# Performance work log

Measured on AMD Instinct MI355X. Metric: run time of the kernel, lower is better.

Reference implementation:

```python
import jax, jax.numpy as jnp
import numpy as np

B, L = 16, 1024
D_MODEL = 384
EXPAND = 2
D_INNER = EXPAND * D_MODEL  # 768
D_STATE = 16
D_CONV = 4
DT_RANK = (D_MODEL + 15) // 16  # 24


def _causal_conv(x, w, b):
    # x: (B,L,Di); w: (Di,K) depthwise kernel; b: (Di,). Causal: pad K-1 on the left.
    K = w.shape[1]
    Lx = x.shape[1]
    xp = jnp.pad(x, ((0, 0), (K - 1, 0), (0, 0)))
    out = sum(xp[:, k:k + Lx, :] * w[:, k] for k in range(K)) + b
    return out


def _selective_scan(u, delta, A, Bm, Cm, Dv):
    # u, delta: (B,L,Di); A: (Di,N); Bm, Cm: (B,L,N); Dv: (Di,)
    def step(h, inp):
        dt, bt, ct, ut = inp  # (B,Di),(B,N),(B,N),(B,Di)
        dA = jnp.exp(dt[..., None] * A)                     # (B,Di,N)
        h = h * dA + (dt * ut)[..., None] * bt[:, None, :]  # (B,Di,N)
        y = jnp.einsum('bdn,bn->bd', h, ct)
        return h, y

    h0 = jnp.zeros((u.shape[0], u.shape[2], A.shape[1]), u.dtype)
    xs = (delta.swapaxes(0, 1), Bm.swapaxes(0, 1), Cm.swapaxes(0, 1), u.swapaxes(0, 1))
    _, ys = jax.lax.scan(step, h0, xs)
    return ys.swapaxes(0, 1) + u * Dv


def _mamba_dir(xz, conv_w, conv_bias, xproj_w, dt_w, dt_b, A_log, Dv):
    xh, z = jnp.split(xz, 2, axis=-1)                 # each (B,L,Di)
    xh = jax.nn.silu(_causal_conv(xh, conv_w, conv_bias))
    dbc = xh @ xproj_w.T                              # (B,L,DT_RANK+2N)
    dt, Bm, Cm = jnp.split(dbc, [DT_RANK, DT_RANK + D_STATE], axis=-1)
    delta = jax.nn.softplus(dt @ dt_w.T + dt_b)       # (B,L,Di)
    A = -jnp.exp(A_log)                               # (Di,N)
    y = _selective_scan(xh, delta, A, Bm, Cm, Dv)
    return y * jax.nn.silu(z)


def setup_inputs():
    key = jax.random.key(0)
    ks = jax.random.split(key, 16)

    def rn(k, shape, s):
        return jax.random.normal(k, shape, dtype=jnp.float32) * s

    A_init = jnp.log(jnp.tile(jnp.arange(1, D_STATE + 1, dtype=jnp.float32), (D_INNER, 1)))
    return dict(
        x=rn(ks[0], (B, L, D_MODEL), 1.0),
        ln_w=jnp.ones((D_MODEL,), jnp.float32),
        ln_b=jnp.zeros((D_MODEL,), jnp.float32),
        in_proj_w=rn(ks[1], (2 * D_INNER, D_MODEL), 0.02),
        out_proj_w=rn(ks[2], (D_MODEL, D_INNER), 0.02),
        conv_w_fwd=rn(ks[3], (D_INNER, D_CONV), 0.2),
        conv_bias_fwd=jnp.zeros((D_INNER,), jnp.float32),
        xproj_w_fwd=rn(ks[4], (DT_RANK + 2 * D_STATE, D_INNER), 0.02),
        dt_w_fwd=rn(ks[5], (D_INNER, DT_RANK), 0.1),
        dt_b_fwd=jnp.full((D_INNER,), -4.0, jnp.float32),
        A_log_fwd=A_init,
        D_fwd=jnp.ones((D_INNER,), jnp.float32),
        conv_w_bwd=rn(ks[6], (D_INNER, D_CONV), 0.2),
        conv_bias_bwd=jnp.zeros((D_INNER,), jnp.float32),
        xproj_w_bwd=rn(ks[7], (DT_RANK + 2 * D_STATE, D_INNER), 0.02),
        dt_w_bwd=rn(ks[8], (D_INNER, DT_RANK), 0.1),
        dt_b_bwd=jnp.full((D_INNER,), -4.0, jnp.float32),
        A_log_bwd=A_init,
        D_bwd=jnp.ones((D_INNER,), jnp.float32),
    )


def reference(x, ln_w, ln_b, in_proj_w, out_proj_w,
              conv_w_fwd, conv_bias_fwd, xproj_w_fwd, dt_w_fwd, dt_b_fwd, A_log_fwd, D_fwd,
              conv_w_bwd, conv_bias_bwd, xproj_w_bwd, dt_w_bwd, dt_b_bwd, A_log_bwd, D_bwd):
    # LayerNorm
    mu = x.mean(-1, keepdims=True)
    var = ((x - mu) ** 2).mean(-1, keepdims=True)
    xn = (x - mu) / jnp.sqrt(var + 1e-5) * ln_w + ln_b
    # Shared input projection -> (B,L,2*Di)
    xz = xn @ in_proj_w.T
    # Forward-direction mamba branch
    out_f = _mamba_dir(xz, conv_w_fwd, conv_bias_fwd, xproj_w_fwd, dt_w_fwd, dt_b_fwd, A_log_fwd, D_fwd)
    # Backward-direction branch on sequence-flipped xz, flipped back (bimamba v2)
    out_r = _mamba_dir(xz[:, ::-1], conv_w_bwd, conv_bias_bwd, xproj_w_bwd, dt_w_bwd, dt_b_bwd, A_log_bwd, D_bwd)[:, ::-1]
    # Output projection + residual (drop_path=0 -> identity)
    return x + (out_f + out_r) @ out_proj_w.T
```

## Files before the change

kernel.cpp:

```cpp
#include <hip/hip_runtime.h>
#include <cstdint>
#include <cstddef>

#define BN_   16
#define LN_   1024
#define DM_   384
#define DI_   768
#define NS_   16
#define RDT_  24
#define NDBC_ 56
#define NDBCP 64
#define NC_   16
#define LC_   64

typedef unsigned short ushortT;
typedef short bf16x8 __attribute__((ext_vector_type(8)));
typedef float f32x4 __attribute__((ext_vector_type(4)));

typedef __attribute__((address_space(3))) uint32_t lds_u32_t;
typedef __attribute__((address_space(1))) const uint32_t glb_u32_t;

static __device__ __forceinline__ void stage16(const void* g, void* lds) {
    __builtin_amdgcn_global_load_lds(
        (glb_u32_t*)(uintptr_t)g,
        (lds_u32_t*)(uint32_t)(uintptr_t)lds,
        16, 0, 0);
}

static __device__ __forceinline__ float silu_f(float x) {
    return x / (1.0f + __expf(-x));
}
static __device__ __forceinline__ float softplus_f(float s) {
    return fmaxf(s, 0.0f) + __logf(1.0f + __expf(-fabsf(s)));
}
static __device__ __forceinline__ ushortT f2bf(float f) {
    union { float f; uint32_t u; } v; v.f = f;
    uint32_t u = v.u;
    uint32_t r = u + 0x7fffu + ((u >> 16) & 1u);
    return (ushortT)(r >> 16);
}
static __device__ __forceinline__ float bf2f(ushortT b) {
    union { uint32_t u; float f; } v; v.u = ((uint32_t)b) << 16;
    return v.f;
}

__global__ __launch_bounds__(256) void wconv_kernel(
    const float* __restrict__ w1, int n1, const float* __restrict__ w2, int n2,
    const float* __restrict__ xwf, const float* __restrict__ xwb,
    const float* __restrict__ dwf, const float* __restrict__ dwb,
    ushortT* __restrict__ o1, ushortT* __restrict__ o2,
    ushortT* __restrict__ oxf, ushortT* __restrict__ oxb,
    ushortT* __restrict__ odf, ushortT* __restrict__ odb)
{
    int i = blockIdx.x * 256 + threadIdx.x;
    if (i < n1) { o1[i] = f2bf(w1[i]); return; }
    i -= n1;
    if (i < n2) { o2[i] = f2bf(w2[i]); return; }
    i -= n2;
    const int nx = NDBCP * DI_;
    if (i < 2 * nx) {
        int which = i >= nx;
        int j = which ? (i - nx) : i;
        int row = j / DI_;
        const float* src = which ? xwb : xwf;
        ushortT* dst = which ? oxb : oxf;
        dst[j] = (row < NDBC_) ? f2bf(src[j]) : (ushortT)0;
        return;
    }
    i -= 2 * nx;
    const int nd = DI_ * 32;
    if (i < 2 * nd) {
        int which = i >= nd;
        int j = which ? (i - nd) : i;
        int row = j >> 5, col = j & 31;
        const float* src = which ? dwb : dwf;
        ushortT* dst = which ? odb : odf;
        dst[j] = (col < RDT_) ? f2bf(src[row * RDT_ + col]) : (ushortT)0;
    }
}

__global__ __launch_bounds__(256) void ln_kernel(
    const float* __restrict__ x, const float* __restrict__ w,
    const float* __restrict__ b, ushortT* __restrict__ xn,
    int row0, int nrows)
{
    int r = blockIdx.x * 4 + (threadIdx.x >> 6);
    if (r >= nrows) return;
    int lane = threadIdx.x & 63;
    const float* xr = x + (size_t)(row0 + r) * DM_;
    float v[6];
    float s = 0.0f;
#pragma unroll
    for (int i = 0; i < 6; i++) { v[i] = xr[lane + 64 * i]; s += v[i]; }
#pragma unroll
    for (int o = 32; o > 0; o >>= 1) s += __shfl_down(s, o, 64);
    s = __shfl(s, 0, 64);
    float mu = s * (1.0f / DM_);
    float q = 0.0f;
#pragma unroll
    for (int i = 0; i < 6; i++) { float d = v[i] - mu; q += d * d; }
#pragma unroll
    for (int o = 32; o > 0; o >>= 1) q += __shfl_down(q, o, 64);
    q = __shfl(q, 0, 64);
    float rstd = rsqrtf(q * (1.0f / DM_) + 1e-5f);
    ushortT* outp = xn + (size_t)r * DM_;
#pragma unroll
    for (int i = 0; i < 6; i++) {
        int c = lane + 64 * i;
        outp[c] = f2bf((v[i] - mu) * rstd * w[c] + b[c]);
    }
}

template <int BM, int BN, int WR, int WC, bool CAT, bool RES, bool OB>
__global__ __launch_bounds__(256) void gemm_mfma(
    const ushortT* __restrict__ Aa, const ushortT* __restrict__ Ab_,
    const ushortT* __restrict__ W, const float* __restrict__ R,
    void* __restrict__ Cv, int M, int N, int Khalf)
{
    constexpr int WTM = BM / WR;
    constexpr int WTN = BN / WC;
    constexpr int FM = WTM / 16;
    constexpr int FN = WTN / 16;
    __shared__ ushortT As[BM * 32];
    __shared__ ushortT Ws[BN * 32];
    int tid = threadIdx.x;
    int bm = blockIdx.x * BM, bn = blockIdx.y * BN;
    int wave = tid >> 6, lane = tid & 63;
    int wm = wave % WR, wn = wave / WR;
    f32x4 acc[FM][FN] = {};
    int Ktot = CAT ? 2 * Khalf : Khalf;
    int lrow = lane >> 2;
    int lk = (lane & 3) * 8;

    for (int k0 = 0; k0 < Ktot; k0 += 32) {
        const ushortT* Asrc = (!CAT || k0 < Khalf) ? Aa : Ab_;
        int ka = (!CAT || k0 < Khalf) ? k0 : (k0 - Khalf);
        __syncthreads();
#pragma unroll
        for (int c = 0; c < BM / 64; c++) {
            int ch = c * 4 + wave;
            int row = ch * 16 + lrow;
            stage16(Asrc + (size_t)(bm + row) * Khalf + ka + lk, &As[ch * 16 * 32]);
        }
#pragma unroll
        for (int c = 0; c < BN / 64; c++) {
            int ch = c * 4 + wave;
            int row = ch * 16 + lrow;
            stage16(W + (size_t)(bn + row) * Khalf + ka + lk, &Ws[ch * 16 * 32]);
        }
        __syncthreads();
        int mb = (wm * WTM + (lane & 15)) * 32 + (lane >> 4) * 8;
        int nb = (wn * WTN + (lane & 15)) * 32 + (lane >> 4) * 8;
        bf16x8 af[FM], bfr[FN];
#pragma unroll
        for (int mi = 0; mi < FM; mi++) af[mi] = *(bf16x8*)&As[mb + mi * 16 * 32];
#pragma unroll
        for (int ni = 0; ni < FN; ni++) bfr[ni] = *(bf16x8*)&Ws[nb + ni * 16 * 32];
#pragma unroll
        for (int mi = 0; mi < FM; mi++)
#pragma unroll
            for (int ni = 0; ni < FN; ni++)
                acc[mi][ni] = __builtin_amdgcn_mfma_f32_16x16x32_bf16(
                    af[mi], bfr[ni], acc[mi][ni], 0, 0, 0);
    }

#pragma unroll
    for (int mi = 0; mi < FM; mi++) {
        int row = bm + wm * WTM + 16 * mi + (lane >> 4) * 4;
#pragma unroll
        for (int ni = 0; ni < FN; ni++) {
            int col = bn + wn * WTN + 16 * ni + (lane & 15);
#pragma unroll
            for (int r = 0; r < 4; r++) {
                size_t o = (size_t)(row + r) * N + col;
                float v = acc[mi][ni][r];
                if (RES) v += R[o];
                if (OB) ((ushortT*)Cv)[o] = f2bf(v);
                else    ((float*)Cv)[o] = v;
            }
        }
    }
}

__global__ __launch_bounds__(256) void conv_kernel(
    const ushortT* __restrict__ XZ,
    const float* __restrict__ wf, const float* __restrict__ bf,
    const float* __restrict__ wb, const float* __restrict__ bb,
    ushortT* __restrict__ XH, int gB)
{
    const int D8 = DI_ / 8;
    int idx = blockIdx.x * 256 + threadIdx.x;
    int perdir = gB * LN_ * D8;
    int dir = 0;
    if (idx >= perdir) { idx -= perdir; dir = 1; }
    int d8 = idx % D8;
    int l = (idx / D8) & (LN_ - 1);
    int b = idx / (D8 * LN_);
    int d = d8 * 8;
    const float* cw = (dir ? wb : wf) + d * 4;
    const float* cb = (dir ? bb : bf) + d;

    float xv[4][8];
#pragma unroll
    for (int k = 0; k < 4; k++) {
        int j = l - 3 + k;
        if (j < 0) {
#pragma unroll
            for (int c = 0; c < 8; c++) xv[k][c] = 0.0f;
        } else {
            int ls = dir ? (LN_ - 1 - j) : j;
            ushort4 v = *(const ushort4*)(XZ + (size_t)(b * LN_ + ls) * (2 * DI_) + d);
            ushort4 v2 = *(const ushort4*)(XZ + (size_t)(b * LN_ + ls) * (2 * DI_) + d + 4);
            xv[k][0] = bf2f(v.x);  xv[k][1] = bf2f(v.y);
            xv[k][2] = bf2f(v.z);  xv[k][3] = bf2f(v.w);
            xv[k][4] = bf2f(v2.x); xv[k][5] = bf2f(v2.y);
            xv[k][6] = bf2f(v2.z); xv[k][7] = bf2f(v2.w);
        }
    }
    ushortT out[8];
#pragma unroll
    for (int c = 0; c < 8; c++) {
        float4 w4 = *(const float4*)(cw + c * 4);
        float s = cb[c];
        s = fmaf(xv[0][c], w4.x, s);
        s = fmaf(xv[1][c], w4.y, s);
        s = fmaf(xv[2][c], w4.z, s);
        s = fmaf(xv[3][c], w4.w, s);
        out[c] = f2bf(silu_f(s));
    }
    ushortT* op = XH + ((size_t)dir * gB * LN_ + (size_t)(b * LN_ + l)) * DI_ + d;
    *(ushort4*)(op + 0) = make_ushort4(out[0], out[1], out[2], out[3]);
    *(ushort4*)(op + 4) = make_ushort4(out[4], out[5], out[6], out[7]);
}

__global__ __launch_bounds__(256) void xproj_mfma(
    const ushortT* __restrict__ XH, const ushortT* __restrict__ Wf,
    const ushortT* __restrict__ Wb, float* __restrict__ Cf,
    float* __restrict__ Cb, ushortT* __restrict__ DT24, int mblocksPerDir)
{
    __shared__ ushortT As[64 * 32];
    __shared__ ushortT Ws[64 * 32];
    int blk = blockIdx.x;
    int dir = blk >= mblocksPerDir;
    const ushortT* W = dir ? Wb : Wf;
    float* C = dir ? Cb : Cf;
    int bmG = blk * 64;
    int bmC = (blk - dir * mblocksPerDir) * 64;
    int tid = threadIdx.x, wave = tid >> 6, lane = tid & 63;
    f32x4 acc[4] = {};
    int lrow = lane >> 2;
    int lk = (lane & 3) * 8;

    for (int k0 = 0; k0 < DI_; k0 += 32) {
        __syncthreads();
        stage16(XH + (size_t)(bmG + wave * 16 + lrow) * DI_ + k0 + lk, &As[wave * 16 * 32]);
        stage16(W + (size_t)(wave * 16 + lrow) * DI_ + k0 + lk, &Ws[wave * 16 * 32]);
        __syncthreads();
        bf16x8 bfr = *(bf16x8*)&Ws[(wave * 16 + (lane & 15)) * 32 + (lane >> 4) * 8];
#pragma unroll
        for (int mi = 0; mi < 4; mi++) {
            bf16x8 af = *(bf16x8*)&As[(mi * 16 + (lane & 15)) * 32 + (lane >> 4) * 8];
            acc[mi] = __builtin_amdgcn_mfma_f32_16x16x32_bf16(af, bfr, acc[mi], 0, 0, 0);
        }
    }
#pragma unroll
    for (int mi = 0; mi < 4; mi++) {
        int row = bmC + 16 * mi + (lane >> 4) * 4;
        int col = wave * 16 + (lane & 15);
#pragma unroll
        for (int r = 0; r < 4; r++)
            C[(size_t)(row + r) * NDBCP + col] = acc[mi][r];
    }
    if (wave < 2) {
        ushortT* dtp = DT24 + (size_t)dir * (size_t)(mblocksPerDir * 64) * 32;
        int col = wave * 16 + (lane & 15);
#pragma unroll
        for (int mi = 0; mi < 4; mi++) {
            int row = bmC + 16 * mi + (lane >> 4) * 4;
#pragma unroll
            for (int r = 0; r < 4; r++)
                dtp[(size_t)(row + r) * 32 + col] =
                    (col < RDT_) ? f2bf(acc[mi][r]) : (ushortT)0;
        }
    }
}

__global__ __launch_bounds__(256) void dtud_kernel(
    const ushortT* __restrict__ DT24, const ushortT* __restrict__ WDtf,
    const ushortT* __restrict__ WDtb,
    const float* __restrict__ dtbf, const float* __restrict__ dtbb,
    const ushortT* __restrict__ XH, uint32_t* __restrict__ UD, int rows)
{
    __shared__ ushortT As[128 * 32];
    __shared__ ushortT Ws[64 * 32];
    int dir = blockIdx.z;
    int bm = blockIdx.x * 128;
    int bn = blockIdx.y * 64;
    const ushortT* A = DT24 + (size_t)dir * rows * 32;
    const ushortT* W = dir ? WDtb : WDtf;
    const float* dtb = dir ? dtbb : dtbf;
    const ushortT* xh = XH + (size_t)dir * rows * DI_;
    uint32_t* ud = UD + (size_t)dir * rows * DI_;
    int tid = threadIdx.x, wave = tid >> 6, lane = tid & 63;
    int lrow = lane >> 2, lk = (lane & 3) * 8;

    stage16(A + (size_t)(bm + wave * 16 + lrow) * 32 + lk, &As[wave * 16 * 32]);
    stage16(A + (size_t)(bm + 64 + wave * 16 + lrow) * 32 + lk, &As[(64 + wave * 16) * 32]);
    stage16(W + (size_t)(bn + wave * 16 + lrow) * 32 + lk, &Ws[wave * 16 * 32]);
    __syncthreads();

    f32x4 acc[2][4] = {};
    bf16x8 bfr[4];
#pragma unroll
    for (int ni = 0; ni < 4; ni++)
        bfr[ni] = *(bf16x8*)&Ws[(ni * 16 + (lane & 15)) * 32 + (lane >> 4) * 8];
#pragma unroll
    for (int mi = 0; mi < 2; mi++) {
        bf16x8 af = *(bf16x8*)&As[(wave * 32 + mi * 16 + (lane & 15)) * 32 + (lane >> 4) * 8];
#pragma unroll
        for (int ni = 0; ni < 4; ni++)
            acc[mi][ni] = __builtin_amdgcn_mfma_f32_16x16x32_bf16(
                af, bfr[ni], acc[mi][ni], 0, 0, 0);
    }
#pragma unroll
    for (int ni = 0; ni < 4; ni++) {
        int d = bn + ni * 16 + (lane & 15);
        float bias = dtb[d];
#pragma unroll
        for (int mi = 0; mi < 2; mi++) {
            int rb = bm + wave * 32 + mi * 16 + (lane >> 4) * 4;
#pragma unroll
            for (int r = 0; r < 4; r++) {
                int row = rb + r;
                float dt = softplus_f(acc[mi][ni][r] + bias);
                float u = bf2f(xh[(size_t)row * DI_ + d]);
                ud[(size_t)row * DI_ + d] =
                    ((uint32_t)f2bf(dt) << 16) | (uint32_t)f2bf(u);
            }
        }
    }
}

__global__ __launch_bounds__(256) void scan1_kernel(
    const uint32_t* __restrict__ UD,
    const float* __restrict__ dbcf, const float* __restrict__ dbcb,
    const float* __restrict__ alogf, const float* __restrict__ alogb,
    uint32_t* __restrict__ SD, int gB)
{
    int bid = blockIdx.x;
    int c = bid % NC_; bid /= NC_;
    int dchunk = bid % 3; bid /= 3;
    int b = bid % gB;
    int dir = bid / gB;
    int d = dchunk * 256 + threadIdx.x;

    const float* dbc  = dir ? dbcb : dbcf;
    const float* alog = dir ? alogb : alogf;

    float An[NS_];
#pragma unroll
    for (int n = 0; n < NS_; n++) An[n] = -__expf(alog[d * NS_ + n]);
    float a1 = An[0];
    bool pk = true;
#pragma unroll
    for (int n = 0; n < NS_; n++)
        pk = pk && (fabsf(An[n] - (float)(n + 1) * a1) <=
                    1e-3f * (float)(n + 1) * fabsf(a1) + 1e-6f);
    pk = (bool)__all((int)pk);

    __shared__ float sB[LC_ * 16];
    int rb = b * LN_ + c * LC_;
    int jb = c * LC_;
    {
        int row = threadIdx.x >> 2, c4 = (threadIdx.x & 3) * 4;
        *(float4*)&sB[row * 16 + c4] =
            *(const float4*)(dbc + (size_t)(rb + row) * NDBCP + RDT_ + c4);
    }
    __syncthreads();

    float h[NS_];
#pragma unroll
    for (int n = 0; n < NS_; n++) h[n] = 0.0f;
    float S = 0.0f;
    const uint32_t* udp = UD + (size_t)((dir * gB + b) * LN_ + jb) * DI_ + d;

    if (pk) {
        uint32_t ud8[8];
#pragma unroll
        for (int i = 0; i < 8; i++) ud8[i] = udp[i * DI_];
        for (int lt = 0; lt < LC_; lt += 8) {
            uint32_t cur[8];
#pragma unroll
            for (int i = 0; i < 8; i++) cur[i] = ud8[i];
            if (lt + 8 < LC_) {
#pragma unroll
                for (int i = 0; i < 8; i++) ud8[i] = udp[(lt + 8 + i) * DI_];
            }
#pragma unroll
            for (int i = 0; i < 8; i++) {
                int lr = lt + i;
                const float4* Bp4 = (const float4*)&sB[lr * 16];
                float4 B0 = Bp4[0], B1 = Bp4[1], B2 = Bp4[2], B3 = Bp4[3];
                float Bv[NS_] = {B0.x, B0.y, B0.z, B0.w, B1.x, B1.y, B1.z, B1.w,
                                 B2.x, B2.y, B2.z, B2.w, B3.x, B3.y, B3.z, B3.w};
                float u = bf2f((ushortT)(cur[i] & 0xffffu));
                float dt = bf2f((ushortT)(cur[i] >> 16));
                S += dt;
                float du = dt * u;
                float q1 = __expf(dt * a1);
                float q2 = q1 * q1, q4 = q2 * q2, q8 = q4 * q4;
                float p2 = q2, p3 = q2 * q1, p5 = q4 * q1, p6 = q4 * q2, p7 = q4 * p3;
                float pw[NS_] = {q1, p2, p3, q4, p5, p6, p7, q8,
                                 q8 * q1, q8 * p2, q8 * p3, q8 * q4,
                                 q8 * p5, q8 * p6, q8 * p7, q8 * q8};
#pragma unroll
                for (int n = 0; n < NS_; n++)
                    h[n] = fmaf(h[n], pw[n], du * Bv[n]);
            }
        }
        float q1 = __expf(S * a1);
        float q2 = q1 * q1, q4 = q2 * q2, q8 = q4 * q4;
        float p2 = q2, p3 = q2 * q1, p5 = q4 * q1, p6 = q4 * q2, p7 = q4 * p3;
        float pw[NS_] = {q1, p2, p3, q4, p5, p6, p7, q8,
                         q8 * q1, q8 * p2, q8 * p3, q8 * q4,
                         q8 * p5, q8 * p6, q8 * p7, q8 * q8};
        int si = (((dir * gB + b) * NC_ + c) * DI_ + d) * NS_;
#pragma unroll
        for (int n = 0; n < NS_; n++)
            SD[si + n] = ((uint32_t)f2bf(pw[n]) << 16) | (uint32_t)f2bf(h[n]);
    } else {
        for (int lr = 0; lr < LC_; lr++) {
            const float* rowp = &sB[lr * 16];
            uint32_t udv = udp[lr * DI_];
            float u = bf2f((ushortT)(udv & 0xffffu));
            float dt = bf2f((ushortT)(udv >> 16));
            S += dt;
            float du = dt * u;
#pragma unroll
            for (int n = 0; n < NS_; n++)
                h[n] = fmaf(h[n], __expf(dt * An[n]), du * rowp[n]);
        }
        int si = (((dir * gB + b) * NC_ + c) * DI_ + d) * NS_;
#pragma unroll
        for (int n = 0; n < NS_; n++)
            SD[si + n] = ((uint32_t)f2bf(__expf(An[n] * S)) << 16) |
                         (uint32_t)f2bf(h[n]);
    }
}

__global__ __launch_bounds__(256) void scan2_kernel(
    const uint32_t* __restrict__ SD, ushortT* __restrict__ hin, int gB)
{
    int e = blockIdx.x * 256 + threadIdx.x;
    int n = e & 15; int e2 = e >> 4;
    int d = e2 % DI_; e2 /= DI_;
    int b = e2 % gB; int dir = e2 / gB;
    int base = (((dir * gB + b) * NC_) * DI_ + d) * NS_ + n;
    float h = 0.0f;
    const int cs = DI_ * NS_;
    for (int c = 0; c < NC_; c++) {
        int idx = base + c * cs;
        uint32_t sd = SD[idx];
        hin[idx] = f2bf(h);
        h = fmaf(h, bf2f((ushortT)(sd >> 16)), bf2f((ushortT)(sd & 0xffffu)));
    }
}

__global__ __launch_bounds__(256) void scan3_kernel(
    const uint32_t* __restrict__ UD, const ushortT* __restrict__ XZ,
    const float* __restrict__ dbcf, const float* __restrict__ dbcb,
    const float* __restrict__ alogf, const float* __restrict__ dvf,
    const float* __restrict__ alogb, const float* __restrict__ dvb,
    const ushortT* __restrict__ hin,
    ushortT* __restrict__ yf, ushortT* __restrict__ yb, int gB)
{
    int bid = blockIdx.x;
    int c = bid % NC_; bid /= NC_;
    int dchunk = bid % 3; bid /= 3;
    int b = bid % gB;
    int dir = bid / gB;
    int d = dchunk * 256 + threadIdx.x;

    const float* dbc  = dir ? dbcb : dbcf;
    const float* alog = dir ? alogb : alogf;
    float Dd          = (dir ? dvb : dvf)[d];
    ushortT* y        = dir ? yb : yf;

    float An[NS_];
#pragma unroll
    for (int n = 0; n < NS_; n++) An[n] = -__expf(alog[d * NS_ + n]);
    float a1 = An[0];
    bool pk = true;
#pragma unroll
    for (int n = 0; n < NS_; n++)
        pk = pk && (fabsf(An[n] - (float)(n + 1) * a1) <=
                    1e-3f * (float)(n + 1) * fabsf(a1) + 1e-6f);
    pk = (bool)__all((int)pk);

    __shared__ float sBC[LC_ * 32];
    int rb = b * LN_ + c * LC_;
    int jb = c * LC_;
#pragma unroll
    for (int i = 0; i < 2; i++) {
        int idx = threadIdx.x + 256 * i;
        int row = idx >> 3, c4 = (idx & 7) * 4;
        *(float4*)&sBC[row * 32 + c4] =
            *(const float4*)(dbc + (size_t)(rb + row) * NDBCP + RDT_ + c4);
    }
    __syncthreads();

    int si = (((dir * gB + b) * NC_ + c) * DI_ + d) * NS_;
    float h[NS_];
#pragma unroll
    for (int n = 0; n < NS_; n++) h[n] = bf2f(hin[si + n]);
    const uint32_t* udp = UD + (size_t)((dir * gB + b) * LN_ + jb) * DI_ + d;

    if (pk) {
        uint32_t ud8[8];
        ushortT z8[8];
#pragma unroll
        for (int i = 0; i < 8; i++) {
            ud8[i] = udp[i * DI_];
            int j = jb + i;
            int lo = dir ? (LN_ - 1 - j) : j;
            z8[i] = XZ[(size_t)(b * LN_ + lo) * (2 * DI_) + DI_ + d];
        }
        for (int lt = 0; lt < LC_; lt += 8) {
            uint32_t cud[8];
            ushortT cz[8];
#pragma unroll
            for (int i = 0; i < 8; i++) { cud[i] = ud8[i]; cz[i] = z8[i]; }
            if (lt + 8 < LC_) {
#pragma unroll
                for (int i = 0; i < 8; i++) {
                    ud8[i] = udp[(lt + 8 + i) * DI_];
                    int j = jb + lt + 8 + i;
                    int lo = dir ? (LN_ - 1 - j) : j;
                    z8[i] = XZ[(size_t)(b * LN_ + lo) * (2 * DI_) + DI_ + d];
                }
            }
#pragma unroll
            for (int i = 0; i < 8; i++) {
                int lr = lt + i;
                const float4* rp4 = (const float4*)&sBC[lr * 32];
                float4 B0 = rp4[0], B1 = rp4[1], B2 = rp4[2], B3 = rp4[3];
                float4 C0 = rp4[4], C1 = rp4[5], C2 = rp4[6], C3 = rp4[7];
                float Bv[NS_] = {B0.x, B0.y, B0.z, B0.w, B1.x, B1.y, B1.z, B1.w,
                                 B2.x, B2.y, B2.z, B2.w, B3.x, B3.y, B3.z, B3.w};
                float Cw[NS_] = {C0.x, C0.y, C0.z, C0.w, C1.x, C1.y, C1.z, C1.w,
                                 C2.x, C2.y, C2.z, C2.w, C3.x, C3.y, C3.z, C3.w};
                float u = bf2f((ushortT)(cud[i] & 0xffffu));
                float dt = bf2f((ushortT)(cud[i] >> 16));
                float du = dt * u;
                float q1 = __expf(dt * a1);
                float q2 = q1 * q1, q4 = q2 * q2, q8 = q4 * q4;
                float p2 = q2, p3 = q2 * q1, p5 = q4 * q1, p6 = q4 * q2, p7 = q4 * p3;
                float pw[NS_] = {q1, p2, p3, q4, p5, p6, p7, q8,
                                 q8 * q1, q8 * p2, q8 * p3, q8 * q4,
                                 q8 * p5, q8 * p6, q8 * p7, q8 * q8};
                float y0 = 0.f, y1 = 0.f, y2 = 0.f, y3 = 0.f;
#pragma unroll
                for (int n = 0; n < NS_; n += 4) {
                    h[n + 0] = fmaf(h[n + 0], pw[n + 0], du * Bv[n + 0]);
                    h[n + 1] = fmaf(h[n + 1], pw[n + 1], du * Bv[n + 1]);
                    h[n + 2] = fmaf(h[n + 2], pw[n + 2], du * Bv[n + 2]);
                    h[n + 3] = fmaf(h[n + 3], pw[n + 3], du * Bv[n + 3]);
                    y0 = fmaf(h[n + 0], Cw[n + 0], y0);
                    y1 = fmaf(h[n + 1], Cw[n + 1], y1);
                    y2 = fmaf(h[n + 2], Cw[n + 2], y2);
                    y3 = fmaf(h[n + 3], Cw[n + 3], y3);
                }
                float yv = ((y0 + y1) + (y2 + y3)) + u * Dd;
                int j = jb + lr;
                int lo = dir ? (LN_ - 1 - j) : j;
                float z = bf2f(cz[i]);
                y[(b * LN_ + lo) * DI_ + d] = f2bf(yv * silu_f(z));
            }
        }
    } else {
        for (int lr = 0; lr < LC_; lr++) {
            const float* rowp = &sBC[lr * 32];
            uint32_t ud = udp[lr * DI_];
            float u = bf2f((ushortT)(ud & 0xffffu));
            float dt = bf2f((ushortT)(ud >> 16));
            float du = dt * u;
            float y0 = 0.f, y1 = 0.f, y2 = 0.f, y3 = 0.f;
#pragma unroll
            for (int n = 0; n < NS_; n += 4) {
                h[n + 0] = fmaf(h[n + 0], __expf(dt * An[n + 0]), du * rowp[n + 0]);
                h[n + 1] = fmaf(h[n + 1], __expf(dt * An[n + 1]), du * rowp[n + 1]);
                h[n + 2] = fmaf(h[n + 2], __expf(dt * An[n + 2]), du * rowp[n + 2]);
                h[n + 3] = fmaf(h[n + 3], __expf(dt * An[n + 3]), du * rowp[n + 3]);
                y0 = fmaf(h[n + 0], rowp[16 + n + 0], y0);
                y1 = fmaf(h[n + 1], rowp[16 + n + 1], y1);
                y2 = fmaf(h[n + 2], rowp[16 + n + 2], y2);
                y3 = fmaf(h[n + 3], rowp[16 + n + 3], y3);
            }
            float yv = ((y0 + y1) + (y2 + y3)) + u * Dd;
            int j = jb + lr;
            int lo = dir ? (LN_ - 1 - j) : j;
            float z = bf2f(XZ[(size_t)(b * LN_ + lo) * (2 * DI_) + DI_ + d]);
            y[(b * LN_ + lo) * DI_ + d] = f2bf(yv * silu_f(z));
        }
    }
}

extern "C" void kernel_launch(void* const* d_in, const int* in_sizes, int n_in,
                              void* d_out, int out_size, void* d_ws, size_t ws_size,
                              hipStream_t stream)
{
    const float* x         = (const float*)d_in[0];
    const float* ln_w      = (const float*)d_in[1];
    const float* ln_b      = (const float*)d_in[2];
    const float* in_proj_w = (const float*)d_in[3];
    const float* out_proj_w= (const float*)d_in[4];
    const float* conv_wf   = (const float*)d_in[5];
    const float* conv_bf   = (const float*)d_in[6];
    const float* xproj_f   = (const float*)d_in[7];
    const float* dt_wf     = (const float*)d_in[8];
    const float* dt_bf     = (const float*)d_in[9];
    const float* alog_f    = (const float*)d_in[10];
    const float* dv_f      = (const float*)d_in[11];
    const float* conv_wb   = (const float*)d_in[12];
    const float* conv_bb   = (const float*)d_in[13];
    const float* xproj_b   = (const float*)d_in[14];
    const float* dt_wb     = (const float*)d_in[15];
    const float* dt_bb     = (const float*)d_in[16];
    const float* alog_b    = (const float*)d_in[17];
    const float* dv_b      = (const float*)d_in[18];
    float* outp = (float*)d_out;

    const int n_w1 = 2 * DI_ * DM_;
    const int n_w2 = DM_ * DI_;
    const int n_wx = NDBCP * DI_;
    const int n_wd = DI_ * 32;

    uint8_t* base = (uint8_t*)d_ws;
    size_t off = 0;
    auto alloc = [&](size_t nbytes) {
        uint8_t* r = base + off;
        off = (off + nbytes + 255) & ~(size_t)255;
        return r;
    };
    ushortT* WbIn  = (ushortT*)alloc((size_t)n_w1 * 2);
    ushortT* WbOut = (ushortT*)alloc((size_t)n_w2 * 2);
    ushortT* WbXf  = (ushortT*)alloc((size_t)n_wx * 2);
    ushortT* WbXb  = (ushortT*)alloc((size_t)n_wx * 2);
    ushortT* WbDtf = (ushortT*)alloc((size_t)n_wd * 2);
    ushortT* WbDtb = (ushortT*)alloc((size_t)n_wd * 2);
    size_t fixed_bytes = off;

    size_t per_b_bytes = 21ull * 1024 * 1024;
    int g = BN_;
    while (g > 1 && fixed_bytes + (size_t)g * per_b_bytes + (1ull << 20) > ws_size) g >>= 1;

    wconv_kernel<<<(n_w1 + n_w2 + 2 * n_wx + 2 * n_wd + 255) / 256, 256, 0, stream>>>(
        in_proj_w, n_w1, out_proj_w, n_w2, xproj_f, xproj_b, dt_wf, dt_wb,
        WbIn, WbOut, WbXf, WbXb, WbDtf, WbDtb);

    for (int b0 = 0; b0 < BN_; b0 += g) {
        int rows = g * LN_;
        off = fixed_bytes;
        ushortT* XNb  = (ushortT*)alloc((size_t)rows * DM_ * 2);
        ushortT* XZ   = (ushortT*)alloc((size_t)rows * 2 * DI_ * 2);
        ushortT* XH   = (ushortT*)alloc((size_t)2 * rows * DI_ * 2);
        float* DBCf   = (float*)alloc((size_t)rows * NDBCP * 4);
        float* DBCb   = (float*)alloc((size_t)rows * NDBCP * 4);
        ushortT* DT24 = (ushortT*)alloc((size_t)2 * rows * 32 * 2);
        uint32_t* UD  = (uint32_t*)alloc((size_t)2 * rows * DI_ * 4);
        size_t st_n   = (size_t)2 * g * NC_ * DI_ * NS_;
        uint32_t* SD  = (uint32_t*)alloc(st_n * 4);
        ushortT* HIN  = (ushortT*)alloc(st_n * 2);
        ushortT* Yf   = (ushortT*)alloc((size_t)rows * DI_ * 2);
        ushortT* Yb   = (ushortT*)alloc((size_t)rows * DI_ * 2);
        int row0 = b0 * LN_;

        ln_kernel<<<rows / 4, 256, 0, stream>>>(x, ln_w, ln_b, XNb, row0, rows);

        gemm_mfma<128, 128, 2, 2, false, false, true>
            <<<dim3(rows / 128, (2 * DI_) / 128), 256, 0, stream>>>(
            XNb, nullptr, WbIn, nullptr, XZ, rows, 2 * DI_, DM_);

        conv_kernel<<<(2 * rows * (DI_ / 8)) / 256, 256, 0, stream>>>(
            XZ, conv_wf, conv_bf, conv_wb, conv_bb, XH, g);

        xproj_mfma<<<2 * (rows / 64), 256, 0, stream>>>(
            XH, WbXf, WbXb, DBCf, DBCb, DT24, rows / 64);

        dtud_kernel<<<dim3(rows / 128, DI_ / 64, 2), 256, 0, stream>>>(
            DT24, WbDtf, WbDtb, dt_bf, dt_bb, XH, UD, rows);

        scan1_kernel<<<2 * g * 3 * NC_, 256, 0, stream>>>(
            UD, DBCf, DBCb, alog_f, alog_b, SD, g);

        scan2_kernel<<<(2 * g * DI_ * NS_) / 256, 256, 0, stream>>>(SD, HIN, g);

        scan3_kernel<<<2 * g * 3 * NC_, 256, 0, stream>>>(
            UD, XZ, DBCf, DBCb, alog_f, dv_f, alog_b, dv_b,
            HIN, Yf, Yb, g);

        gemm_mfma<64, 128, 1, 4, true, true, false>
            <<<dim3(rows / 64, DM_ / 128), 256, 0, stream>>>(
            Yf, Yb, WbOut, x + (size_t)row0 * DM_,
            outp + (size_t)row0 * DM_, rows, DM_, DI_);
    }
}
```

Baseline: 486.2 us.

## Fuse dt projection into xproj kernel and double-buffer scan prefetch

Merges the dt low-rank projection and the softplus/UD packing into the xproj GEMM kernel. The dt24 activations now stay in LDS instead of going through a global DT24 buffer, which saves one launch and a global round trip. The fused kernel loops over all 768 output columns per 64-row block with a single MFMA per tile, so each block does more serial work and the grid has less parallelism for the dt stage. Separately, scan1 and scan3 now prefetch two groups of UD/z values ahead instead of one, to hide memory latency at the cost of extra registers.

```diff
diff --git a/kernel.cpp b/kernel.cpp
--- a/kernel.cpp
+++ b/kernel.cpp
@@ -233,16 +233,21 @@
     *(ushort4*)(op + 4) = make_ushort4(out[4], out[5], out[6], out[7]);
 }
 
-__global__ __launch_bounds__(256) void xproj_mfma(
+__global__ __launch_bounds__(256) void xprojdt_mfma(
     const ushortT* __restrict__ XH, const ushortT* __restrict__ Wf,
-    const ushortT* __restrict__ Wb, float* __restrict__ Cf,
-    float* __restrict__ Cb, ushortT* __restrict__ DT24, int mblocksPerDir)
+    const ushortT* __restrict__ Wb,
+    const ushortT* __restrict__ WDtf, const ushortT* __restrict__ WDtb,
+    const float* __restrict__ dtbf, const float* __restrict__ dtbb,
+    float* __restrict__ Cf, float* __restrict__ Cb,
+    uint32_t* __restrict__ UD, int mblocksPerDir)
 {
     __shared__ ushortT As[64 * 32];
     __shared__ ushortT Ws[64 * 32];
     int blk = blockIdx.x;
     int dir = blk >= mblocksPerDir;
-    const ushortT* W = dir ? Wb : Wf;
+    const ushortT* W   = dir ? Wb : Wf;
+    const ushortT* WDt = dir ? WDtb : WDtf;
+    const float* dtb   = dir ? dtbb : dtbf;
     float* C = dir ? Cb : Cf;
     int bmG = blk * 64;
     int bmC = (blk - dir * mblocksPerDir) * 64;
@@ -271,70 +276,42 @@
         for (int r = 0; r < 4; r++)
             C[(size_t)(row + r) * NDBCP + col] = acc[mi][r];
     }
+
+    __syncthreads();
     if (wave < 2) {
-        ushortT* dtp = DT24 + (size_t)dir * (size_t)(mblocksPerDir * 64) * 32;
         int col = wave * 16 + (lane & 15);
 #pragma unroll
         for (int mi = 0; mi < 4; mi++) {
-            int row = bmC + 16 * mi + (lane >> 4) * 4;
+            int row = 16 * mi + (lane >> 4) * 4;
 #pragma unroll
             for (int r = 0; r < 4; r++)
-                dtp[(size_t)(row + r) * 32 + col] =
-                    (col < RDT_) ? f2bf(acc[mi][r]) : (ushortT)0;
-        }
-    }
-}
-
-__global__ __launch_bounds__(256) void dtud_kernel(
-    const ushortT* __restrict__ DT24, const ushortT* __restrict__ WDtf,
-    const ushortT* __restrict__ WDtb,
-    const float* __restrict__ dtbf, const float* __restrict__ dtbb,
-    const ushortT* __restrict__ XH, uint32_t* __restrict__ UD, int rows)
-{
-    __shared__ ushortT As[128 * 32];
-    __shared__ ushortT Ws[64 * 32];
-    int dir = blockIdx.z;
-    int bm = blockIdx.x * 128;
-    int bn = blockIdx.y * 64;
-    const ushortT* A = DT24 + (size_t)dir * rows * 32;
-    const ushortT* W = dir ? WDtb : WDtf;
-    const float* dtb = dir ? dtbb : dtbf;
-    const ushortT* xh = XH + (size_t)dir * rows * DI_;
-    uint32_t* ud = UD + (size_t)dir * rows * DI_;
-    int tid = threadIdx.x, wave = tid >> 6, lane = tid & 63;
-    int lrow = lane >> 2, lk = (lane & 3) * 8;
-
-    stage16(A + (size_t)(bm + wave * 16 + lrow) * 32 + lk, &As[wave * 16 * 32]);
-    stage16(A + (size_t)(bm + 64 + wave * 16 + lrow) * 32 + lk, &As[(64 + wave * 16) * 32]);
-    stage16(W + (size_t)(bn + wave * 16 + lrow) * 32 + lk, &Ws[wave * 16 * 32]);
+                As[(row + r) * 32 + col] = f2bf(acc[mi][r]);
+        }
+    }
     __syncthreads();
-
-    f32x4 acc[2][4] = {};
-    bf16x8 bfr[4];
-#pragma unroll
-    for (int ni = 0; ni < 4; ni++)
-        bfr[ni] = *(bf16x8*)&Ws[(ni * 16 + (lane & 15)) * 32 + (lane >> 4) * 8];
-#pragma unroll
-    for (int mi = 0; mi < 2; mi++) {
-        bf16x8 af = *(bf16x8*)&As[(wave * 32 + mi * 16 + (lane & 15)) * 32 + (lane >> 4) * 8];
-#pragma unroll
-        for (int ni = 0; ni < 4; ni++)
-            acc[mi][ni] = __builtin_amdgcn_mfma_f32_16x16x32_bf16(
-                af, bfr[ni], acc[mi][ni], 0, 0, 0);
-    }
-#pragma unroll
-    for (int ni = 0; ni < 4; ni++) {
-        int d = bn + ni * 16 + (lane & 15);
+    bf16x8 afd[4];
+#pragma unroll
+    for (int mi = 0; mi < 4; mi++)
+        afd[mi] = *(bf16x8*)&As[(mi * 16 + (lane & 15)) * 32 + (lane >> 4) * 8];
+
+    for (int nt = 0; nt < DI_ / 64; nt++) {
+        __syncthreads();
+        stage16(WDt + (size_t)(nt * 64 + wave * 16 + lrow) * 32 + lk, &Ws[wave * 16 * 32]);
+        __syncthreads();
+        bf16x8 bfr = *(bf16x8*)&Ws[(wave * 16 + (lane & 15)) * 32 + (lane >> 4) * 8];
+        int d = nt * 64 + wave * 16 + (lane & 15);
         float bias = dtb[d];
 #pragma unroll
-        for (int mi = 0; mi < 2; mi++) {
-            int rb = bm + wave * 32 + mi * 16 + (lane >> 4) * 4;
+        for (int mi = 0; mi < 4; mi++) {
+            f32x4 z = {0.f, 0.f, 0.f, 0.f};
+            f32x4 a2 = __builtin_amdgcn_mfma_f32_16x16x32_bf16(afd[mi], bfr, z, 0, 0, 0);
+            int rowb = bmG + 16 * mi + (lane >> 4) * 4;
 #pragma unroll
             for (int r = 0; r < 4; r++) {
-                int row = rb + r;
-                float dt = softplus_f(acc[mi][ni][r] + bias);
-                float u = bf2f(xh[(size_t)row * DI_ + d]);
-                ud[(size_t)row * DI_ + d] =
+                int row = rowb + r;
+                float dt = softplus_f(a2[r] + bias);
+                float u = bf2f(XH[(size_t)row * DI_ + d]);
+                UD[(size_t)row * DI_ + d] =
                     ((uint32_t)f2bf(dt) << 16) | (uint32_t)f2bf(u);
             }
         }
@@ -385,17 +362,22 @@
     const uint32_t* udp = UD + (size_t)((dir * gB + b) * LN_ + jb) * DI_ + d;
 
     if (pk) {
-        uint32_t ud8[8];
-#pragma unroll
-        for (int i = 0; i < 8; i++) ud8[i] = udp[i * DI_];
-        for (int lt = 0; lt < LC_; lt += 8) {
+        uint32_t udb[2][8];
+#pragma unroll
+        for (int i = 0; i < 8; i++) udb[0][i] = udp[i * DI_];
+#pragma unroll
+        for (int i = 0; i < 8; i++) udb[1][i] = udp[(8 + i) * DI_];
+        for (int gq = 0; gq < LC_ / 8; gq++) {
+            int p = gq & 1;
             uint32_t cur[8];
 #pragma unroll
-            for (int i = 0; i < 8; i++) cur[i] = ud8[i];
-            if (lt + 8 < LC_) {
-#pragma unroll
-                for (int i = 0; i < 8; i++) ud8[i] = udp[(lt + 8 + i) * DI_];
+            for (int i = 0; i < 8; i++) cur[i] = udb[p][i];
+            if (gq + 2 < LC_ / 8) {
+#pragma unroll
+                for (int i = 0; i < 8; i++)
+                    udb[p][i] = udp[((gq + 2) * 8 + i) * DI_];
             }
+            int lt = gq * 8;
 #pragma unroll
             for (int i = 0; i < 8; i++) {
                 int lr = lt + i;
@@ -516,29 +498,39 @@
     const uint32_t* udp = UD + (size_t)((dir * gB + b) * LN_ + jb) * DI_ + d;
 
     if (pk) {
-        uint32_t ud8[8];
-        ushortT z8[8];
+        uint32_t udb[2][8];
+        ushortT zbf[2][8];
 #pragma unroll
         for (int i = 0; i < 8; i++) {
-            ud8[i] = udp[i * DI_];
+            udb[0][i] = udp[i * DI_];
             int j = jb + i;
             int lo = dir ? (LN_ - 1 - j) : j;
-            z8[i] = XZ[(size_t)(b * LN_ + lo) * (2 * DI_) + DI_ + d];
-        }
-        for (int lt = 0; lt < LC_; lt += 8) {
+            zbf[0][i] = XZ[(size_t)(b * LN_ + lo) * (2 * DI_) + DI_ + d];
+        }
+#pragma unroll
+        for (int i = 0; i < 8; i++) {
+            udb[1][i] = udp[(8 + i) * DI_];
+            int j = jb + 8 + i;
+            int lo = dir ? (LN_ - 1 - j) : j;
+            zbf[1][i] = XZ[(size_t)(b * LN_ + lo) * (2 * DI_) + DI_ + d];
+        }
+        for (int gq = 0; gq < LC_ / 8; gq++) {
+            int p = gq & 1;
             uint32_t cud[8];
             ushortT cz[8];
 #pragma unroll
-            for (int i = 0; i < 8; i++) { cud[i] = ud8[i]; cz[i] = z8[i]; }
-            if (lt + 8 < LC_) {
+            for (int i = 0; i < 8; i++) { cud[i] = udb[p][i]; cz[i] = zbf[p][i]; }
+            if (gq + 2 < LC_ / 8) {
 #pragma unroll
                 for (int i = 0; i < 8; i++) {
-                    ud8[i] = udp[(lt + 8 + i) * DI_];
-                    int j = jb + lt + 8 + i;
+                    int jj = (gq + 2) * 8 + i;
+                    udb[p][i] = udp[jj * DI_];
+                    int j = jb + jj;
                     int lo = dir ? (LN_ - 1 - j) : j;
-                    z8[i] = XZ[(size_t)(b * LN_ + lo) * (2 * DI_) + DI_ + d];
+                    zbf[p][i] = XZ[(size_t)(b * LN_ + lo) * (2 * DI_) + DI_ + d];
                 }
             }
+            int lt = gq * 8;
 #pragma unroll
             for (int i = 0; i < 8; i++) {
                 int lr = lt + i;
@@ -666,7 +658,6 @@
         ushortT* XH   = (ushortT*)alloc((size_t)2 * rows * DI_ * 2);
         float* DBCf   = (float*)alloc((size_t)rows * NDBCP * 4);
         float* DBCb   = (float*)alloc((size_t)rows * NDBCP * 4);
-        ushortT* DT24 = (ushortT*)alloc((size_t)2 * rows * 32 * 2);
         uint32_t* UD  = (uint32_t*)alloc((size_t)2 * rows * DI_ * 4);
         size_t st_n   = (size_t)2 * g * NC_ * DI_ * NS_;
         uint32_t* SD  = (uint32_t*)alloc(st_n * 4);
@@ -684,11 +675,9 @@
         conv_kernel<<<(2 * rows * (DI_ / 8)) / 256, 256, 0, stream>>>(
             XZ, conv_wf, conv_bf, conv_wb, conv_bb, XH, g);
 
-        xproj_mfma<<<2 * (rows / 64), 256, 0, stream>>>(
-            XH, WbXf, WbXb, DBCf, DBCb, DT24, rows / 64);
-
-        dtud_kernel<<<dim3(rows / 128, DI_ / 64, 2), 256, 0, stream>>>(
-            DT24, WbDtf, WbDtb, dt_bf, dt_bb, XH, UD, rows);
+        xprojdt_mfma<<<2 * (rows / 64), 256, 0, stream>>>(
+            XH, WbXf, WbXb, WbDtf, WbDtb, dt_bf, dt_bb,
+            DBCf, DBCb, UD, rows / 64);
 
         scan1_kernel<<<2 * g * 3 * NC_, 256, 0, stream>>>(
             UD, DBCf, DBCb, alog_f, alog_b, SD, g);
```

Measured after the change: 629.0 us. 29.4% more time.
